# Kernel tuning notes

Measured on AMD Instinct MI355X. Metric: run time of the kernel, lower is better.

## Reference

```python
import jax, jax.numpy as jnp
from jax import lax
import numpy as np

T, B, INPUT_SIZE, HIDDEN, LAYERS, OUT_DIM = 256, 1000, 300, 2, 2, 1


def setup_inputs() -> dict:
    key = jax.random.key(0)
    ks = jax.random.split(key, 12)
    H4 = 4 * HIDDEN
    s = 0.1
    return {
        "x": jax.random.normal(ks[0], (T, B, INPUT_SIZE), dtype=jnp.float32),
        "h0": jnp.zeros((LAYERS, B, HIDDEN), dtype=jnp.float32),
        "c0": jnp.zeros((LAYERS, B, HIDDEN), dtype=jnp.float32),
        "W_ih0": jax.random.normal(ks[1], (H4, INPUT_SIZE), dtype=jnp.float32) * s,
        "W_hh0": jax.random.normal(ks[2], (H4, HIDDEN), dtype=jnp.float32) * s,
        "b_ih0": jax.random.normal(ks[3], (H4,), dtype=jnp.float32) * s,
        "b_hh0": jax.random.normal(ks[4], (H4,), dtype=jnp.float32) * s,
        "W_ih1": jax.random.normal(ks[5], (H4, HIDDEN), dtype=jnp.float32) * s,
        "W_hh1": jax.random.normal(ks[6], (H4, HIDDEN), dtype=jnp.float32) * s,
        "b_ih1": jax.random.normal(ks[7], (H4,), dtype=jnp.float32) * s,
        "b_hh1": jax.random.normal(ks[8], (H4,), dtype=jnp.float32) * s,
        "W_lin": jax.random.normal(ks[9], (OUT_DIM, HIDDEN), dtype=jnp.float32) * s,
        "b_lin": jax.random.normal(ks[10], (OUT_DIM,), dtype=jnp.float32) * s,
    }


def _lstm_layer(x, h0, c0, W_ih, W_hh, b_ih, b_hh):
    # x: [T, B, D_in]; PyTorch gate order i, f, g, o.
    # Precompute input projections for all timesteps at once (one big GEMM).
    xg = jnp.einsum('tbd,gd->tbg', x, W_ih) + (b_ih + b_hh)  # [T, B, 4H]

    def step(carry, xt):
        h, c = carry
        gates = xt + h @ W_hh.T  # [B, 4H]
        i, f, g, o = jnp.split(gates, 4, axis=-1)
        c = jax.nn.sigmoid(f) * c + jax.nn.sigmoid(i) * jnp.tanh(g)
        h = jax.nn.sigmoid(o) * jnp.tanh(c)
        return (h, c), h

    (_, _), ys = lax.scan(step, (h0, c0), xg)
    return ys  # [T, B, H]


def reference(x, h0, c0, W_ih0, W_hh0, b_ih0, b_hh0, W_ih1, W_hh1, b_ih1, b_hh1, W_lin, b_lin):
    y0 = _lstm_layer(x, h0[0], c0[0], W_ih0, W_hh0, b_ih0, b_hh0)   # [T, B, H]
    y1 = _lstm_layer(y0, h0[1], c0[1], W_ih1, W_hh1, b_ih1, b_hh1)  # [T, B, H]
    pred = y1[-1] @ W_lin.T + b_lin  # [B, 1]
    return pred.reshape(-1)          # [B]
```

## Files before the change

kernel.cpp:

```cpp
#include <hip/hip_runtime.h>

#define T_STEPS 256
#define BATCH   1000
#define D_IN    300
#define H4      8
#define NF4     75
#define RPB     128
#define NBLK    2000

#define L2E   1.4426950408889634f
#define L2E2  2.8853900817779268f

__device__ __forceinline__ float fexp2(float x) {
#if __has_builtin(__builtin_amdgcn_exp2f)
    return __builtin_amdgcn_exp2f(x);
#else
    return exp2f(x);
#endif
}
__device__ __forceinline__ float sig2(float x) {
    return __builtin_amdgcn_rcpf(1.0f + fexp2(-x));
}
__device__ __forceinline__ float tanh2(float x) {
    return fmaf(-2.0f, __builtin_amdgcn_rcpf(1.0f + fexp2(x)), 1.0f);
}

__device__ __forceinline__ float dot4acc(float4 a, float4 b, float acc) {
    return fmaf(a.x, b.x, fmaf(a.y, b.y, fmaf(a.z, b.z, fmaf(a.w, b.w, acc))));
}

__global__ __launch_bounds__(256) void xproj_kernel(
    const float* __restrict__ x, const float* __restrict__ W,
    const float* __restrict__ b_ih, const float* __restrict__ b_hh,
    float* __restrict__ xg)
{
    __shared__ __align__(16) float4 ws4[H4 * NF4];

    const int tid = threadIdx.x;
    const float4* __restrict__ w4 = (const float4*)W;
    for (int k = tid; k < H4 * NF4; k += 256)
        ws4[k] = w4[k];
    __syncthreads();

    const int  lane = tid & 3;
    const int  quad = tid >> 2;
    const long row0 = (long)blockIdx.x * RPB + (long)quad * 2;

    const float4* __restrict__ x0 = (const float4*)x + row0 * NF4;
    const float4* __restrict__ x1 = x0 + NF4;

    float acc0[H4], acc1[H4];
#pragma unroll
    for (int g = 0; g < H4; ++g) { acc0[g] = 0.f; acc1[g] = 0.f; }

#pragma unroll 3
    for (int i = 0; i < 18; ++i) {
        const int k = 4 * i + lane;
        float4 xa = x0[k];
        float4 xb = x1[k];
#pragma unroll
        for (int g = 0; g < H4; ++g) {
            float4 wv = ws4[g * NF4 + k];
            acc0[g] = dot4acc(xa, wv, acc0[g]);
            acc1[g] = dot4acc(xb, wv, acc1[g]);
        }
    }
    {
        const int k = 72 + lane;
        if (k < NF4) {
            float4 xa = x0[k];
            float4 xb = x1[k];
#pragma unroll
            for (int g = 0; g < H4; ++g) {
                float4 wv = ws4[g * NF4 + k];
                acc0[g] = dot4acc(xa, wv, acc0[g]);
                acc1[g] = dot4acc(xb, wv, acc1[g]);
            }
        }
    }

#pragma unroll
    for (int g = 0; g < H4; ++g) {
        acc0[g] += __shfl_xor(acc0[g], 1);
        acc0[g] += __shfl_xor(acc0[g], 2);
        acc1[g] += __shfl_xor(acc1[g], 1);
        acc1[g] += __shfl_xor(acc1[g], 2);
    }

    const int   g0 = lane * 2;
    const float b0 = b_ih[g0]     + b_hh[g0];
    const float b1 = b_ih[g0 + 1] + b_hh[g0 + 1];
    const float sc = (lane == 2) ? L2E2 : L2E;

    float2* __restrict__ out2 = (float2*)xg;
    float2 o0 = { (acc0[g0] + b0) * sc, (acc0[g0 + 1] + b1) * sc };
    float2 o1 = { (acc1[g0] + b0) * sc, (acc1[g0 + 1] + b1) * sc };
    out2[row0 * 4 + lane]       = o0;
    out2[(row0 + 1) * 4 + lane] = o1;
}

__global__ __launch_bounds__(64) void lstm_seq_kernel(
    const float* __restrict__ xg,
    const float* __restrict__ h0in, const float* __restrict__ c0in,
    const float* __restrict__ Whh0, const float* __restrict__ Wih1,
    const float* __restrict__ Whh1, const float* __restrict__ bih1,
    const float* __restrict__ bhh1, const float* __restrict__ Wlin,
    const float* __restrict__ blin, float* __restrict__ out)
{
    int b = blockIdx.x * 64 + threadIdx.x;
    bool active = (b < BATCH);
    int bb = active ? b : (BATCH - 1);

    float whh0[H4][2], wih1[H4][2], whh1[H4][2], bias1[H4];
#pragma unroll
    for (int k = 0; k < H4; ++k) {
        float f = (k == 4 || k == 5) ? L2E2 : L2E;
        whh0[k][0] = Whh0[2 * k] * f; whh0[k][1] = Whh0[2 * k + 1] * f;
        wih1[k][0] = Wih1[2 * k] * f; wih1[k][1] = Wih1[2 * k + 1] * f;
        whh1[k][0] = Whh1[2 * k] * f; whh1[k][1] = Whh1[2 * k + 1] * f;
        bias1[k]   = (bih1[k] + bhh1[k]) * f;
    }

    float h0a = h0in[2 * bb],             h0b = h0in[2 * bb + 1];
    float c0a = c0in[2 * bb],             c0b = c0in[2 * bb + 1];
    float h1a = h0in[2 * BATCH + 2 * bb], h1b = h0in[2 * BATCH + 2 * bb + 1];
    float c1a = c0in[2 * BATCH + 2 * bb], c1b = c0in[2 * BATCH + 2 * bb + 1];

    const float4* __restrict__ xp = (const float4*)xg;

    float4 plo[4], phi[4];
#pragma unroll
    for (int t = 0; t < 4; ++t) {
        plo[t] = xp[(t * BATCH + bb) * 2];
        phi[t] = xp[(t * BATCH + bb) * 2 + 1];
    }

    float p[H4];
#pragma unroll
    for (int k = 0; k < H4; ++k)
        p[k] = bias1[k] + h1a * whh1[k][0] + h1b * whh1[k][1];

#pragma unroll 4
    for (int t = 0; t < T_STEPS; ++t) {
        int s = t & 3;
        float4 l4 = plo[s], h4 = phi[s];
        if (t + 4 < T_STEPS) {
            plo[s] = xp[((t + 4) * BATCH + bb) * 2];
            phi[s] = xp[((t + 4) * BATCH + bb) * 2 + 1];
        }
        float xv[H4] = {l4.x, l4.y, l4.z, l4.w, h4.x, h4.y, h4.z, h4.w};

        float gt[H4];
#pragma unroll
        for (int k = 0; k < H4; ++k)
            gt[k] = xv[k] + h0a * whh0[k][0] + h0b * whh0[k][1];
        c0a = sig2(gt[2]) * c0a + sig2(gt[0]) * tanh2(gt[4]);
        c0b = sig2(gt[3]) * c0b + sig2(gt[1]) * tanh2(gt[5]);
        h0a = sig2(gt[6]) * tanh2(c0a * L2E2);
        h0b = sig2(gt[7]) * tanh2(c0b * L2E2);

        float qt[H4];
#pragma unroll
        for (int k = 0; k < H4; ++k)
            qt[k] = p[k] + h0a * wih1[k][0] + h0b * wih1[k][1];
        c1a = sig2(qt[2]) * c1a + sig2(qt[0]) * tanh2(qt[4]);
        c1b = sig2(qt[3]) * c1b + sig2(qt[1]) * tanh2(qt[5]);
        h1a = sig2(qt[6]) * tanh2(c1a * L2E2);
        h1b = sig2(qt[7]) * tanh2(c1b * L2E2);

#pragma unroll
        for (int k = 0; k < H4; ++k)
            p[k] = bias1[k] + h1a * whh1[k][0] + h1b * whh1[k][1];
    }

    if (active)
        out[b] = h1a * Wlin[0] + h1b * Wlin[1] + blin[0];
}

extern "C" void kernel_launch(void* const* d_in, const int* in_sizes, int n_in,
                              void* d_out, int out_size, void* d_ws, size_t ws_size,
                              hipStream_t stream) {
    const float* x      = (const float*)d_in[0];
    const float* h0     = (const float*)d_in[1];
    const float* c0     = (const float*)d_in[2];
    const float* W_ih0  = (const float*)d_in[3];
    const float* W_hh0  = (const float*)d_in[4];
    const float* b_ih0  = (const float*)d_in[5];
    const float* b_hh0  = (const float*)d_in[6];
    const float* W_ih1  = (const float*)d_in[7];
    const float* W_hh1  = (const float*)d_in[8];
    const float* b_ih1  = (const float*)d_in[9];
    const float* b_hh1  = (const float*)d_in[10];
    const float* W_lin  = (const float*)d_in[11];
    const float* b_lin  = (const float*)d_in[12];
    float* out = (float*)d_out;
    float* xg  = (float*)d_ws;

    xproj_kernel<<<NBLK, 256, 0, stream>>>(x, W_ih0, b_ih0, b_hh0, xg);
    lstm_seq_kernel<<<(BATCH + 63) / 64, 64, 0, stream>>>(
        xg, h0, c0, W_hh0, W_ih1, W_hh1, b_ih1, b_hh1, W_lin, b_lin, out);
}
```

Measured before the change: 555.8 us.

## Split each LSTM batch element across two lanes, one per hidden unit

The sequential LSTM kernel now assigns two threads per batch element, each owning one hidden unit's four gates, and exchanges the partner's h value through a DPP lane swap. To match, the projection kernel writes its gate outputs interleaved so that each lane loads a single float4 per step. This halves the serial per-thread transcendental chain and doubles the wavefront count for the latency-bound recurrence. In exchange it adds a cross-lane swap on the critical path each step and uses scattered scalar stores in the projection kernel.

```diff
diff --git a/kernel.cpp b/kernel.cpp
--- a/kernel.cpp
+++ b/kernel.cpp
@@ -29,6 +29,15 @@
     return fmaf(a.x, b.x, fmaf(a.y, b.y, fmaf(a.z, b.z, fmaf(a.w, b.w, acc))));
 }
 
+__device__ __forceinline__ float swap1(float x) {
+#if __has_builtin(__builtin_amdgcn_mov_dpp)
+    return __int_as_float(
+        __builtin_amdgcn_mov_dpp(__float_as_int(x), 0xB1, 0xF, 0xF, true));
+#else
+    return __shfl_xor(x, 1);
+#endif
+}
+
 __global__ __launch_bounds__(256) void xproj_kernel(
     const float* __restrict__ x, const float* __restrict__ W,
     const float* __restrict__ b_ih, const float* __restrict__ b_hh,
@@ -87,16 +96,14 @@
         acc1[g] += __shfl_xor(acc1[g], 2);
     }
 
-    const int   g0 = lane * 2;
-    const float b0 = b_ih[g0]     + b_hh[g0];
-    const float b1 = b_ih[g0 + 1] + b_hh[g0 + 1];
+    const float b0 = b_ih[2 * lane]     + b_hh[2 * lane];
+    const float b1 = b_ih[2 * lane + 1] + b_hh[2 * lane + 1];
     const float sc = (lane == 2) ? L2E2 : L2E;
 
-    float2* __restrict__ out2 = (float2*)xg;
-    float2 o0 = { (acc0[g0] + b0) * sc, (acc0[g0 + 1] + b1) * sc };
-    float2 o1 = { (acc1[g0] + b0) * sc, (acc1[g0 + 1] + b1) * sc };
-    out2[row0 * 4 + lane]       = o0;
-    out2[(row0 + 1) * 4 + lane] = o1;
+    xg[row0 * 8 + lane]           = (acc0[2 * lane]     + b0) * sc;
+    xg[row0 * 8 + 4 + lane]       = (acc0[2 * lane + 1] + b1) * sc;
+    xg[(row0 + 1) * 8 + lane]     = (acc1[2 * lane]     + b0) * sc;
+    xg[(row0 + 1) * 8 + 4 + lane] = (acc1[2 * lane + 1] + b1) * sc;
 }
 
 __global__ __launch_bounds__(64) void lstm_seq_kernel(
@@ -107,74 +114,75 @@
     const float* __restrict__ bhh1, const float* __restrict__ Wlin,
     const float* __restrict__ blin, float* __restrict__ out)
 {
-    int b = blockIdx.x * 64 + threadIdx.x;
-    bool active = (b < BATCH);
-    int bb = active ? b : (BATCH - 1);
-
-    float whh0[H4][2], wih1[H4][2], whh1[H4][2], bias1[H4];
-#pragma unroll
-    for (int k = 0; k < H4; ++k) {
-        float f = (k == 4 || k == 5) ? L2E2 : L2E;
-        whh0[k][0] = Whh0[2 * k] * f; whh0[k][1] = Whh0[2 * k + 1] * f;
-        wih1[k][0] = Wih1[2 * k] * f; wih1[k][1] = Wih1[2 * k + 1] * f;
-        whh1[k][0] = Whh1[2 * k] * f; whh1[k][1] = Whh1[2 * k + 1] * f;
-        bias1[k]   = (bih1[k] + bhh1[k]) * f;
-    }
-
-    float h0a = h0in[2 * bb],             h0b = h0in[2 * bb + 1];
-    float c0a = c0in[2 * bb],             c0b = c0in[2 * bb + 1];
-    float h1a = h0in[2 * BATCH + 2 * bb], h1b = h0in[2 * BATCH + 2 * bb + 1];
-    float c1a = c0in[2 * BATCH + 2 * bb], c1b = c0in[2 * BATCH + 2 * bb + 1];
-
-    const float4* __restrict__ xp = (const float4*)xg;
-
-    float4 plo[4], phi[4];
-#pragma unroll
-    for (int t = 0; t < 4; ++t) {
-        plo[t] = xp[(t * BATCH + bb) * 2];
-        phi[t] = xp[(t * BATCH + bb) * 2 + 1];
-    }
-
-    float p[H4];
-#pragma unroll
-    for (int k = 0; k < H4; ++k)
-        p[k] = bias1[k] + h1a * whh1[k][0] + h1b * whh1[k][1];
+    const int gid   = blockIdx.x * 64 + threadIdx.x;
+    const int e_raw = gid >> 1;
+    const int u     = gid & 1;
+    const bool wr   = (e_raw < BATCH) && (u == 0);
+    const int  e    = (e_raw < BATCH) ? e_raw : (BATCH - 1);
+
+    float wa0[4], wb0[4], wa1i[4], wb1i[4], wa1h[4], wb1h[4], bs1[4];
+#pragma unroll
+    for (int s = 0; s < 4; ++s) {
+        const int   row = 2 * s + u;
+        const float f   = (s == 2) ? L2E2 : L2E;
+        wa0[s]  = Whh0[row * 2 + u]       * f;
+        wb0[s]  = Whh0[row * 2 + (1 - u)] * f;
+        wa1i[s] = Wih1[row * 2 + u]       * f;
+        wb1i[s] = Wih1[row * 2 + (1 - u)] * f;
+        wa1h[s] = Whh1[row * 2 + u]       * f;
+        wb1h[s] = Whh1[row * 2 + (1 - u)] * f;
+        bs1[s]  = (bih1[row] + bhh1[row]) * f;
+    }
+
+    float h0 = h0in[2 * e + u];
+    float c0 = c0in[2 * e + u];
+    float h1 = h0in[2 * BATCH + 2 * e + u];
+    float c1 = c0in[2 * BATCH + 2 * e + u];
+
+    const float4* __restrict__ xq = (const float4*)xg;
+    float4 pre[4];
+#pragma unroll
+    for (int t = 0; t < 4; ++t)
+        pre[t] = xq[((long)t * BATCH + e) * 2 + u];
+
+    float h1o = swap1(h1);
+    float p[4];
+#pragma unroll
+    for (int s = 0; s < 4; ++s)
+        p[s] = bs1[s] + h1 * wa1h[s] + h1o * wb1h[s];
 
 #pragma unroll 4
     for (int t = 0; t < T_STEPS; ++t) {
-        int s = t & 3;
-        float4 l4 = plo[s], h4 = phi[s];
-        if (t + 4 < T_STEPS) {
-            plo[s] = xp[((t + 4) * BATCH + bb) * 2];
-            phi[s] = xp[((t + 4) * BATCH + bb) * 2 + 1];
-        }
-        float xv[H4] = {l4.x, l4.y, l4.z, l4.w, h4.x, h4.y, h4.z, h4.w};
-
-        float gt[H4];
-#pragma unroll
-        for (int k = 0; k < H4; ++k)
-            gt[k] = xv[k] + h0a * whh0[k][0] + h0b * whh0[k][1];
-        c0a = sig2(gt[2]) * c0a + sig2(gt[0]) * tanh2(gt[4]);
-        c0b = sig2(gt[3]) * c0b + sig2(gt[1]) * tanh2(gt[5]);
-        h0a = sig2(gt[6]) * tanh2(c0a * L2E2);
-        h0b = sig2(gt[7]) * tanh2(c0b * L2E2);
-
-        float qt[H4];
-#pragma unroll
-        for (int k = 0; k < H4; ++k)
-            qt[k] = p[k] + h0a * wih1[k][0] + h0b * wih1[k][1];
-        c1a = sig2(qt[2]) * c1a + sig2(qt[0]) * tanh2(qt[4]);
-        c1b = sig2(qt[3]) * c1b + sig2(qt[1]) * tanh2(qt[5]);
-        h1a = sig2(qt[6]) * tanh2(c1a * L2E2);
-        h1b = sig2(qt[7]) * tanh2(c1b * L2E2);
-
-#pragma unroll
-        for (int k = 0; k < H4; ++k)
-            p[k] = bias1[k] + h1a * whh1[k][0] + h1b * whh1[k][1];
-    }
-
-    if (active)
-        out[b] = h1a * Wlin[0] + h1b * Wlin[1] + blin[0];
+        const int sl = t & 3;
+        const float4 xv = pre[sl];
+        if (t + 4 < T_STEPS)
+            pre[sl] = xq[((long)(t + 4) * BATCH + e) * 2 + u];
+
+        const float h0o = swap1(h0);
+        const float gi = xv.x + h0 * wa0[0] + h0o * wb0[0];
+        const float gf = xv.y + h0 * wa0[1] + h0o * wb0[1];
+        const float gg = xv.z + h0 * wa0[2] + h0o * wb0[2];
+        const float go = xv.w + h0 * wa0[3] + h0o * wb0[3];
+        c0 = sig2(gf) * c0 + sig2(gi) * tanh2(gg);
+        h0 = sig2(go) * tanh2(c0 * L2E2);
+
+        const float h0n = swap1(h0);
+        const float qi = p[0] + h0 * wa1i[0] + h0n * wb1i[0];
+        const float qf = p[1] + h0 * wa1i[1] + h0n * wb1i[1];
+        const float qg = p[2] + h0 * wa1i[2] + h0n * wb1i[2];
+        const float qo = p[3] + h0 * wa1i[3] + h0n * wb1i[3];
+        c1 = sig2(qf) * c1 + sig2(qi) * tanh2(qg);
+        h1 = sig2(qo) * tanh2(c1 * L2E2);
+
+        const float h1n = swap1(h1);
+#pragma unroll
+        for (int s = 0; s < 4; ++s)
+            p[s] = bs1[s] + h1 * wa1h[s] + h1n * wb1h[s];
+    }
+
+    const float h1b = swap1(h1);
+    if (wr)
+        out[e] = h1 * Wlin[0] + h1b * Wlin[1] + blin[0];
 }
 
 extern "C" void kernel_launch(void* const* d_in, const int* in_sizes, int n_in,
@@ -197,6 +205,6 @@
     float* xg  = (float*)d_ws;
 
     xproj_kernel<<<NBLK, 256, 0, stream>>>(x, W_ih0, b_ih0, b_hh0, xg);
-    lstm_seq_kernel<<<(BATCH + 63) / 64, 64, 0, stream>>>(
+    lstm_seq_kernel<<<(2 * BATCH + 63) / 64, 64, 0, stream>>>(
         xg, h0, c0, W_hh0, W_ih1, W_hh1, b_ih1, b_hh1, W_lin, b_lin, out);
 }
```

After: 498.5 us. 1.12x faster.
